# Kernel optimization log

Measured on AMD Instinct MI355X. Metric: run time of the kernel, lower is better.

The kernel has to match this reference:

```python
import jax, jax.numpy as jnp
import numpy as np
import math

B, L, D, H = 16, 512, 128, 8


def setup_inputs() -> dict:
    key = jax.random.key(0)
    ks = jax.random.split(key, 10)
    xavier = lambda k, shp: jax.random.normal(k, shp, jnp.float32) * math.sqrt(2.0 / (shp[0] + shp[1]))
    inp = {
        "x": jax.random.normal(ks[0], (B, L, D), jnp.float32),
        "W_q": xavier(ks[1], (H * D, D)),
        "b_q": jnp.zeros((H * D,), jnp.float32),
        "W_k": xavier(ks[2], (H * D, D)),
        "b_k": jnp.zeros((H * D,), jnp.float32),
        "W_v": xavier(ks[3], (H * D, D)),
        "b_v": jnp.zeros((H * D,), jnp.float32),
        "W_o": xavier(ks[4], (D, H * D)),
        "b_o": jnp.zeros((D,), jnp.float32),
        "pad_mask": jax.random.randint(ks[5], (B, L, L), 0, 2).astype(bool),
        "batch_size": B,
        "max_len": L,
    }
    return inp


def reference(x, W_q, b_q, W_k, b_k, W_v, b_v, W_o, b_o, pad_mask, batch_size, max_len):
    # project: [B, L, D] -> [B, L, H*D] -> head-major [H*B, L, D]
    def proj(W, b):
        y = jnp.einsum('bld,ed->ble', x, W) + b          # [B, L, H*D]
        y = y.reshape(batch_size, max_len, H, D)
        return y.transpose(2, 0, 1, 3).reshape(H * batch_size, max_len, D)

    q = proj(W_q, b_q)
    k = proj(W_k, b_k)
    v = proj(W_v, b_v)

    scores = jnp.einsum('nqd,nkd->nqk', q, k)            # [H*B, L, L]
    mask = jnp.tile(pad_mask, (H, 1, 1))                 # repeat(n_heads,1,1)
    # faithful quirk: mask BEFORE scaling, softmax over QUERY axis (dim=1)
    scores = jnp.where(mask, -1e9, scores) / math.sqrt(D)
    attn = jax.nn.softmax(scores, axis=1)
    att = jnp.einsum('nqk,nkd->nqd', attn, v)            # [H*B, L, D]
    # faithful quirk: torch .view from (H*B, L, D) to (B, L, H*D)
    att = att.reshape(batch_size, max_len, H * D)
    out = jnp.einsum('ble,de->bld', att, W_o) + b_o      # [B, L, D]
    return out
```

## Files before the change

kernel.cpp:

```cpp
#include <hip/hip_runtime.h>

#define B_  16
#define L_  512
#define D_  128
#define H_  8
#define HD_ 1024
#define NH_ 128
#define M_  8192

typedef unsigned short u16;
typedef __attribute__((ext_vector_type(8))) short s16x8;
typedef __attribute__((ext_vector_type(4))) float f32x4;

__device__ __forceinline__ float bf2f(u16 u) {
    union { unsigned u; float f; } x; x.u = ((unsigned)u) << 16; return x.f;
}
__device__ __forceinline__ u16 f2bf(float f) {
    unsigned u = __float_as_uint(f);
    return (u16)((u + 0x7FFFu + ((u >> 16) & 1u)) >> 16);
}

__device__ __forceinline__ void mfma_bt64(const u16* __restrict__ A, int lda,
                                          const u16* __restrict__ B, int ldb,
                                          int K, int lane, f32x4 acc[4][4]) {
    const int mr = lane & 15, quad = lane >> 4;
    for (int k0 = 0; k0 < K; k0 += 32) {
        s16x8 av[4], bv[4];
#pragma unroll
        for (int i = 0; i < 4; i++)
            av[i] = *(const s16x8*)(A + (size_t)(i * 16 + mr) * lda + k0 + quad * 8);
#pragma unroll
        for (int j = 0; j < 4; j++)
            bv[j] = *(const s16x8*)(B + (size_t)(j * 16 + mr) * ldb + k0 + quad * 8);
#pragma unroll
        for (int i = 0; i < 4; i++)
#pragma unroll
            for (int j = 0; j < 4; j++)
                acc[i][j] = __builtin_amdgcn_mfma_f32_16x16x32_bf16(av[i], bv[j], acc[i][j], 0, 0, 0);
    }
}

__global__ void k0_detect(const unsigned int* __restrict__ pad,
                          const unsigned int* __restrict__ xw,
                          int* __restrict__ flags) {
    __shared__ int sMask, sCnt;
    if (threadIdx.x == 0) { sMask = 0; sCnt = 0; }
    __syncthreads();
    int bad = 0;
#pragma unroll
    for (int i = 0; i < 4; i++) {
        unsigned u = pad[threadIdx.x * 4 + i];
        bad |= (u > 1u) ? 1 : 0;
    }
    int cnt = 0;
#pragma unroll
    for (int i = 0; i < 16; i++) {
        unsigned w = xw[threadIdx.x * 16 + i];
        unsigned e = (w >> 7) & 0xFFu;
        cnt += (e >= 100u && e <= 131u) ? 1 : 0;
    }
    if (bad) atomicOr(&sMask, 1);
    atomicAdd(&sCnt, cnt);
    __syncthreads();
    if (threadIdx.x == 0) {
        flags[0] = (sCnt > 2048) ? 1 : 0;
        flags[1] = sMask;
    }
}

#define PREP_TOT 1576064
__global__ __launch_bounds__(256) void kprep_conv(
    const void* x, const void* Wq, const void* bq, const void* Wk, const void* bk,
    const void* Wv, const void* bv, const void* Wo, const void* bo,
    const int* __restrict__ flags,
    u16* xb, u16* Wqb, u16* Wkb, u16* Wvb, u16* Wob,
    u16* bqb, u16* bkb, u16* bvb, u16* bob) {
    int gid = blockIdx.x * 256 + threadIdx.x;
    if (gid >= PREP_TOT) return;
    const int dt = flags[0];
    const void* src; u16* dst; int off;
    if      (gid < 1048576) { src = x;  dst = xb;  off = gid; }
    else if (gid < 1179648) { src = Wq; dst = Wqb; off = gid - 1048576; }
    else if (gid < 1310720) { src = Wk; dst = Wkb; off = gid - 1179648; }
    else if (gid < 1441792) { src = Wv; dst = Wvb; off = gid - 1310720; }
    else if (gid < 1572864) { src = Wo; dst = Wob; off = gid - 1441792; }
    else if (gid < 1573888) { src = bq; dst = bqb; off = gid - 1572864; }
    else if (gid < 1574912) { src = bk; dst = bkb; off = gid - 1573888; }
    else if (gid < 1575936) { src = bv; dst = bvb; off = gid - 1574912; }
    else                    { src = bo; dst = bob; off = gid - 1575936; }
    dst[off] = dt ? ((const u16*)src)[off] : f2bf(((const float*)src)[off]);
}

__global__ __launch_bounds__(256) void kprep_mask(const void* __restrict__ pad,
                                                  const int* __restrict__ flags,
                                                  unsigned* __restrict__ mb,
                                                  float* __restrict__ colsum) {
    int w = blockIdx.x * 256 + threadIdx.x;
    if (w < NH_ * L_) colsum[w] = 0.0f;
    unsigned m = 0;
    if (flags[1]) {
        const uint4* p = (const uint4*)pad + (size_t)w * 2;
        uint4 a = p[0], b = p[1];
        unsigned ws[8] = {a.x, a.y, a.z, a.w, b.x, b.y, b.z, b.w};
#pragma unroll
        for (int i = 0; i < 8; i++) {
            unsigned v = ws[i];
            m |= ((v & 0xFFu)        ? 1u : 0u) << (i * 4)
               | ((v & 0xFF00u)     ? 1u : 0u) << (i * 4 + 1)
               | ((v & 0xFF0000u)   ? 1u : 0u) << (i * 4 + 2)
               | ((v & 0xFF000000u) ? 1u : 0u) << (i * 4 + 3);
        }
    } else {
        const uint4* p = (const uint4*)pad + (size_t)w * 8;
#pragma unroll
        for (int i = 0; i < 8; i++) {
            uint4 v = p[i];
            m |= (v.x ? 1u : 0u) << (i * 4)
               | (v.y ? 1u : 0u) << (i * 4 + 1)
               | (v.z ? 1u : 0u) << (i * 4 + 2)
               | (v.w ? 1u : 0u) << (i * 4 + 3);
        }
    }
    mb[w] = m;
}

__global__ __launch_bounds__(256) void k1_proj(
    const u16* __restrict__ xb,
    const u16* __restrict__ Wqb, const u16* __restrict__ Wkb, const u16* __restrict__ Wvb,
    const u16* __restrict__ bqb, const u16* __restrict__ bkb, const u16* __restrict__ bvb,
    u16* __restrict__ qb, u16* __restrict__ kb, u16* __restrict__ vtb) {
    const int h  = blockIdx.x;
    const int m0 = blockIdx.y * 128;
    const int z  = blockIdx.z;
    const u16* W    = (z == 0) ? Wqb : (z == 1) ? Wkb : Wvb;
    const u16* bias = (z == 0) ? bqb : (z == 1) ? bkb : bvb;

    const int lane = threadIdx.x & 63, wave = threadIdx.x >> 6;
    const int wr = wave >> 1, wc = wave & 1;
    const int mr = lane & 15, quad = lane >> 4;

    f32x4 acc[4][4];
#pragma unroll
    for (int i = 0; i < 4; i++)
#pragma unroll
        for (int j = 0; j < 4; j++) acc[i][j] = (f32x4){0.f, 0.f, 0.f, 0.f};

    mfma_bt64(xb + (size_t)(m0 + wr * 64) * D_, D_,
              W + (size_t)(h * 128 + wc * 64) * D_, D_, D_, lane, acc);

    __shared__ __align__(16) u16 T[128][144];
#pragma unroll
    for (int i = 0; i < 4; i++)
#pragma unroll
        for (int j = 0; j < 4; j++) {
            int col = wc * 64 + j * 16 + mr;
            float bv_ = bf2f(bias[h * 128 + col]);
#pragma unroll
            for (int r = 0; r < 4; r++)
                T[wr * 64 + i * 16 + quad * 4 + r][col] = f2bf(acc[i][j][r] + bv_);
        }
    __syncthreads();

    const int bb = m0 >> 9, l0 = m0 & 511;
    const int t = threadIdx.x;
    if (z < 2) {
        u16* out = z ? kb : qb;
        int row = t >> 1, c0 = (t & 1) * 64;
        u16* dst = out + ((size_t)(h * B_ + bb) * L_ + l0 + row) * D_ + c0;
#pragma unroll
        for (int c = 0; c < 64; c += 8)
            *(uint4*)(dst + c) = *(const uint4*)&T[row][c0 + c];
    } else {
        int d = t >> 1, lc0 = (t & 1) * 64;
        u16* dst = vtb + ((size_t)(h * B_ + bb) * D_ + d) * L_ + l0 + lc0;
#pragma unroll
        for (int c = 0; c < 64; c += 8) {
            u16 tmp[8];
#pragma unroll
            for (int s = 0; s < 8; s++) tmp[s] = T[lc0 + c + s][d];
            *(uint4*)(dst + c) = *(const uint4*)tmp;
        }
    }
}

__global__ __launch_bounds__(256, 4) void k2_scores(
    const u16* __restrict__ qb, const u16* __restrict__ kb,
    const unsigned* __restrict__ mbits,
    u16* __restrict__ sb, float* __restrict__ colsum) {
    const int qt = blockIdx.x >> 2, kt = blockIdx.x & 3;
    const int n  = blockIdx.y;
    const int bb = n & (B_ - 1);
    const int lane = threadIdx.x & 63, wave = threadIdx.x >> 6;
    const int wr = wave >> 1, wc = wave & 1;
    const int mr = lane & 15, quad = lane >> 4;
    const float rs = 0.08838834764831845f;

    __shared__ __align__(16) u16 T[128][136];
    __shared__ float CS[2][128];
    __shared__ unsigned MW[128][4];

    {
        int t = threadIdx.x;
        int q = t >> 1, w2 = (t & 1) * 2;
        const unsigned* src = mbits + ((size_t)(bb << 9) + qt * 128 + q) * 16 + kt * 4 + w2;
        uint2 v = *(const uint2*)src;
        MW[q][w2] = v.x; MW[q][w2 + 1] = v.y;
    }

    f32x4 acc[4][4];
#pragma unroll
    for (int i = 0; i < 4; i++)
#pragma unroll
        for (int j = 0; j < 4; j++) acc[i][j] = (f32x4){0.f, 0.f, 0.f, 0.f};

    mfma_bt64(qb + ((size_t)n * L_ + qt * 128 + wr * 64) * D_, D_,
              kb + ((size_t)n * L_ + kt * 128 + wc * 64) * D_, D_, D_, lane, acc);
    __syncthreads();

    float cs[4] = {0.f, 0.f, 0.f, 0.f};
#pragma unroll
    for (int j = 0; j < 4; j++) {
        const int wsel = wc * 2 + (j >> 1);
        const int bit  = ((j & 1) << 4) + mr;
#pragma unroll
        for (int i = 0; i < 4; i++)
#pragma unroll
            for (int r = 0; r < 4; r++) {
                int ql = wr * 64 + i * 16 + quad * 4 + r;
                unsigned w = MW[ql][wsel];
                float e = ((w >> bit) & 1u) ? 0.f : __expf(acc[i][j][r] * rs);
                cs[j] += e;
                T[ql][wc * 64 + j * 16 + mr] = f2bf(e);
            }
    }
#pragma unroll
    for (int j = 0; j < 4; j++) {
        cs[j] += __shfl_xor(cs[j], 16);
        cs[j] += __shfl_xor(cs[j], 32);
    }
    if (quad == 0) {
#pragma unroll
        for (int j = 0; j < 4; j++) CS[wr][wc * 64 + j * 16 + mr] = cs[j];
    }
    __syncthreads();
    {
        int t = threadIdx.x, row = t >> 1, c0 = (t & 1) * 64;
        u16* dst = sb + ((size_t)n * L_ + qt * 128 + row) * L_ + kt * 128 + c0;
#pragma unroll
        for (int c = 0; c < 64; c += 8)
            *(uint4*)(dst + c) = *(const uint4*)&T[row][c0 + c];
    }
    if (threadIdx.x < 128)
        atomicAdd(&colsum[(size_t)n * L_ + kt * 128 + threadIdx.x],
                  CS[0][threadIdx.x] + CS[1][threadIdx.x]);
}

__global__ __launch_bounds__(256) void k3_vscale(u16* __restrict__ vtb,
                                                 const float* __restrict__ colsum) {
    int idx = blockIdx.x * 256 + threadIdx.x;
    int n = idx >> 13;
    int rem = idx & 8191;
    int d = rem >> 6;
    int kg = (rem & 63) << 3;
    u16* p = vtb + ((size_t)n * D_ + d) * L_ + kg;
    uint4 v = *(const uint4*)p;
    float cv[8];
    *(float4*)&cv[0] = *(const float4*)(colsum + (size_t)n * L_ + kg);
    *(float4*)&cv[4] = *(const float4*)(colsum + (size_t)n * L_ + kg + 4);
    u16* u = (u16*)&v;
#pragma unroll
    for (int s = 0; s < 8; s++) u[s] = f2bf(bf2f(u[s]) / cv[s]);
    *(uint4*)p = v;
}

__global__ __launch_bounds__(256) void k4_av(
    const u16* __restrict__ sb, const u16* __restrict__ vtb,
    u16* __restrict__ att) {
    const int q0 = blockIdx.x * 128;
    const int n  = blockIdx.y;
    const int lane = threadIdx.x & 63, wave = threadIdx.x >> 6;
    const int wr = wave >> 1, wc = wave & 1;
    const int mr = lane & 15, quad = lane >> 4;

    f32x4 acc[4][4];
#pragma unroll
    for (int i = 0; i < 4; i++)
#pragma unroll
        for (int j = 0; j < 4; j++) acc[i][j] = (f32x4){0.f, 0.f, 0.f, 0.f};

    mfma_bt64(sb + ((size_t)n * L_ + q0 + wr * 64) * L_, L_,
              vtb + ((size_t)n * D_ + wc * 64) * L_, L_, L_, lane, acc);

    __shared__ __align__(16) u16 T[128][136];
#pragma unroll
    for (int i = 0; i < 4; i++)
#pragma unroll
        for (int j = 0; j < 4; j++) {
            int col = wc * 64 + j * 16 + mr;
#pragma unroll
            for (int r = 0; r < 4; r++)
                T[wr * 64 + i * 16 + quad * 4 + r][col] = f2bf(acc[i][j][r]);
        }
    __syncthreads();
    int t = threadIdx.x, row = t >> 1, c0 = (t & 1) * 64;
    u16* dst = att + ((size_t)n * L_ + q0 + row) * D_ + c0;
#pragma unroll
    for (int c = 0; c < 64; c += 8)
        *(uint4*)(dst + c) = *(const uint4*)&T[row][c0 + c];
}

__global__ __launch_bounds__(256) void k5_out(
    const u16* __restrict__ att, const u16* __restrict__ Wob,
    const u16* __restrict__ bob, const int* __restrict__ flags,
    void* __restrict__ out) {
    const int dt = flags[0];
    const int m0 = blockIdx.x * 32;
    const int lane = threadIdx.x & 63, wave = threadIdx.x >> 6;
    const int mr = lane & 15, quad = lane >> 4;

    f32x4 acc[2][2];
#pragma unroll
    for (int i = 0; i < 2; i++)
#pragma unroll
        for (int j = 0; j < 2; j++) acc[i][j] = (f32x4){0.f, 0.f, 0.f, 0.f};

    const u16* A  = att + (size_t)m0 * HD_;
    const u16* Bw = Wob + (size_t)(wave * 32) * HD_;
    for (int k0 = 0; k0 < HD_; k0 += 32) {
        s16x8 av[2], bv[2];
#pragma unroll
        for (int i = 0; i < 2; i++)
            av[i] = *(const s16x8*)(A + (size_t)(i * 16 + mr) * HD_ + k0 + quad * 8);
#pragma unroll
        for (int j = 0; j < 2; j++)
            bv[j] = *(const s16x8*)(Bw + (size_t)(j * 16 + mr) * HD_ + k0 + quad * 8);
#pragma unroll
        for (int i = 0; i < 2; i++)
#pragma unroll
            for (int j = 0; j < 2; j++)
                acc[i][j] = __builtin_amdgcn_mfma_f32_16x16x32_bf16(av[i], bv[j], acc[i][j], 0, 0, 0);
    }

    __shared__ __align__(16) float Tf[32][132];
#pragma unroll
    for (int i = 0; i < 2; i++)
#pragma unroll
        for (int j = 0; j < 2; j++) {
            int col = wave * 32 + j * 16 + mr;
            float bv_ = bf2f(bob[col]);
#pragma unroll
            for (int r = 0; r < 4; r++)
                Tf[i * 16 + quad * 4 + r][col] = acc[i][j][r] + bv_;
        }
    __syncthreads();
    int t = threadIdx.x, row = t >> 3, cg = (t & 7) * 16;
    size_t base = (size_t)(m0 + row) * D_ + cg;
    if (dt) {
        u16* o = (u16*)out;
        u16 tmp[16];
#pragma unroll
        for (int s = 0; s < 16; s++) tmp[s] = f2bf(Tf[row][cg + s]);
        *(uint4*)(o + base)     = *(const uint4*)&tmp[0];
        *(uint4*)(o + base + 8) = *(const uint4*)&tmp[8];
    } else {
        float* o = (float*)out;
#pragma unroll
        for (int c = 0; c < 16; c += 4)
            *(float4*)(o + base + c) = *(const float4*)&Tf[row][cg + c];
    }
}

extern "C" void kernel_launch(void* const* d_in, const int* in_sizes, int n_in,
                              void* d_out, int out_size, void* d_ws, size_t ws_size,
                              hipStream_t stream) {
    (void)in_sizes; (void)n_in; (void)out_size; (void)ws_size;
    const void* x  = d_in[0];
    const void* Wq = d_in[1]; const void* bq = d_in[2];
    const void* Wk = d_in[3]; const void* bk = d_in[4];
    const void* Wv = d_in[5]; const void* bv = d_in[6];
    const void* Wo = d_in[7]; const void* bo = d_in[8];
    const void* pad = d_in[9];

    char* p = (char*)d_ws;
    auto alloc = [&](size_t bytes) { char* r = p; p += (bytes + 255) & ~(size_t)255; return r; };
    int*  flags = (int*)alloc(256);
    u16*  xb   = (u16*)alloc(2097152);
    u16*  Wqb  = (u16*)alloc(262144);
    u16*  Wkb  = (u16*)alloc(262144);
    u16*  Wvb  = (u16*)alloc(262144);
    u16*  Wob  = (u16*)alloc(262144);
    u16*  bqb  = (u16*)alloc(2048);
    u16*  bkb  = (u16*)alloc(2048);
    u16*  bvb  = (u16*)alloc(2048);
    u16*  bob  = (u16*)alloc(256);
    unsigned* mbits = (unsigned*)alloc(524288);
    float* colsum = (float*)alloc(262144);
    u16*  qb   = (u16*)alloc(16777216);
    u16*  kb   = (u16*)alloc(16777216);
    u16*  vtb  = (u16*)alloc(16777216);
    u16*  sb   = (u16*)alloc(67108864);
    u16*  att  = qb;

    k0_detect<<<1, 256, 0, stream>>>((const unsigned*)pad, (const unsigned*)x, flags);
    kprep_conv<<<(PREP_TOT + 255) / 256, 256, 0, stream>>>(
        x, Wq, bq, Wk, bk, Wv, bv, Wo, bo, flags,
        xb, Wqb, Wkb, Wvb, Wob, bqb, bkb, bvb, bob);
    kprep_mask<<<512, 256, 0, stream>>>(pad, flags, mbits, colsum);
    k1_proj<<<dim3(8, 64, 3), 256, 0, stream>>>(
        xb, Wqb, Wkb, Wvb, bqb, bkb, bvb, qb, kb, vtb);
    k2_scores<<<dim3(16, NH_), 256, 0, stream>>>(qb, kb, mbits, sb, colsum);
    k3_vscale<<<4096, 256, 0, stream>>>(vtb, colsum);
    k4_av<<<dim3(4, NH_), 256, 0, stream>>>(sb, vtb, att);
    k5_out<<<256, 256, 0, stream>>>(att, Wob, bob, flags, d_out);
}
```

Before: 253.4 us.

## Fuse V column scaling into AV kernel and vectorize prep conversion

Removes the separate k3_vscale pass. The softmax denominator reciprocal is now applied to the score operand inside the AV matmul loop, which is equivalent because it indexes the reduction axis. The prep conversion kernel processes 8 elements per thread with vector loads and stores. The projection grid axes are swapped, which changes block scheduling order. Scaling in k4 is repeated across q tiles and adds ALU work in the inner loop, and rounding differs slightly.

New measurement: 244.9 us. -3.4%, faster.

```diff
diff --git a/kernel.cpp b/kernel.cpp
--- a/kernel.cpp
+++ b/kernel.cpp
@@ -69,6 +69,7 @@
 }
 
 #define PREP_TOT 1576064
+#define PREP_V   197008
 __global__ __launch_bounds__(256) void kprep_conv(
     const void* x, const void* Wq, const void* bq, const void* Wk, const void* bk,
     const void* Wv, const void* bv, const void* Wo, const void* bo,
@@ -76,19 +77,28 @@
     u16* xb, u16* Wqb, u16* Wkb, u16* Wvb, u16* Wob,
     u16* bqb, u16* bkb, u16* bvb, u16* bob) {
     int gid = blockIdx.x * 256 + threadIdx.x;
-    if (gid >= PREP_TOT) return;
+    if (gid >= PREP_V) return;
+    int e0 = gid * 8;
     const int dt = flags[0];
     const void* src; u16* dst; int off;
-    if      (gid < 1048576) { src = x;  dst = xb;  off = gid; }
-    else if (gid < 1179648) { src = Wq; dst = Wqb; off = gid - 1048576; }
-    else if (gid < 1310720) { src = Wk; dst = Wkb; off = gid - 1179648; }
-    else if (gid < 1441792) { src = Wv; dst = Wvb; off = gid - 1310720; }
-    else if (gid < 1572864) { src = Wo; dst = Wob; off = gid - 1441792; }
-    else if (gid < 1573888) { src = bq; dst = bqb; off = gid - 1572864; }
-    else if (gid < 1574912) { src = bk; dst = bkb; off = gid - 1573888; }
-    else if (gid < 1575936) { src = bv; dst = bvb; off = gid - 1574912; }
-    else                    { src = bo; dst = bob; off = gid - 1575936; }
-    dst[off] = dt ? ((const u16*)src)[off] : f2bf(((const float*)src)[off]);
+    if      (e0 < 1048576) { src = x;  dst = xb;  off = e0; }
+    else if (e0 < 1179648) { src = Wq; dst = Wqb; off = e0 - 1048576; }
+    else if (e0 < 1310720) { src = Wk; dst = Wkb; off = e0 - 1179648; }
+    else if (e0 < 1441792) { src = Wv; dst = Wvb; off = e0 - 1310720; }
+    else if (e0 < 1572864) { src = Wo; dst = Wob; off = e0 - 1441792; }
+    else if (e0 < 1573888) { src = bq; dst = bqb; off = e0 - 1572864; }
+    else if (e0 < 1574912) { src = bk; dst = bkb; off = e0 - 1573888; }
+    else if (e0 < 1575936) { src = bv; dst = bvb; off = e0 - 1574912; }
+    else                   { src = bo; dst = bob; off = e0 - 1575936; }
+    if (dt) {
+        *(uint4*)(dst + off) = *(const uint4*)((const u16*)src + off);
+    } else {
+        const float* s = (const float*)src + off;
+        float4 a = *(const float4*)s, b = *(const float4*)(s + 4);
+        u16 tmp[8] = {f2bf(a.x), f2bf(a.y), f2bf(a.z), f2bf(a.w),
+                      f2bf(b.x), f2bf(b.y), f2bf(b.z), f2bf(b.w)};
+        *(uint4*)(dst + off) = *(const uint4*)tmp;
+    }
 }
 
 __global__ __launch_bounds__(256) void kprep_mask(const void* __restrict__ pad,
@@ -129,8 +139,8 @@
     const u16* __restrict__ Wqb, const u16* __restrict__ Wkb, const u16* __restrict__ Wvb,
     const u16* __restrict__ bqb, const u16* __restrict__ bkb, const u16* __restrict__ bvb,
     u16* __restrict__ qb, u16* __restrict__ kb, u16* __restrict__ vtb) {
-    const int h  = blockIdx.x;
-    const int m0 = blockIdx.y * 128;
+    const int h  = blockIdx.y;
+    const int m0 = blockIdx.x * 128;
     const int z  = blockIdx.z;
     const u16* W    = (z == 0) ? Wqb : (z == 1) ? Wkb : Wvb;
     const u16* bias = (z == 0) ? bqb : (z == 1) ? bkb : bvb;
@@ -255,27 +265,9 @@
                   CS[0][threadIdx.x] + CS[1][threadIdx.x]);
 }
 
-__global__ __launch_bounds__(256) void k3_vscale(u16* __restrict__ vtb,
-                                                 const float* __restrict__ colsum) {
-    int idx = blockIdx.x * 256 + threadIdx.x;
-    int n = idx >> 13;
-    int rem = idx & 8191;
-    int d = rem >> 6;
-    int kg = (rem & 63) << 3;
-    u16* p = vtb + ((size_t)n * D_ + d) * L_ + kg;
-    uint4 v = *(const uint4*)p;
-    float cv[8];
-    *(float4*)&cv[0] = *(const float4*)(colsum + (size_t)n * L_ + kg);
-    *(float4*)&cv[4] = *(const float4*)(colsum + (size_t)n * L_ + kg + 4);
-    u16* u = (u16*)&v;
-#pragma unroll
-    for (int s = 0; s < 8; s++) u[s] = f2bf(bf2f(u[s]) / cv[s]);
-    *(uint4*)p = v;
-}
-
 __global__ __launch_bounds__(256) void k4_av(
     const u16* __restrict__ sb, const u16* __restrict__ vtb,
-    u16* __restrict__ att) {
+    const float* __restrict__ colsum, u16* __restrict__ att) {
     const int q0 = blockIdx.x * 128;
     const int n  = blockIdx.y;
     const int lane = threadIdx.x & 63, wave = threadIdx.x >> 6;
@@ -288,8 +280,37 @@
 #pragma unroll
         for (int j = 0; j < 4; j++) acc[i][j] = (f32x4){0.f, 0.f, 0.f, 0.f};
 
-    mfma_bt64(sb + ((size_t)n * L_ + q0 + wr * 64) * L_, L_,
-              vtb + ((size_t)n * D_ + wc * 64) * L_, L_, L_, lane, acc);
+    const u16* A   = sb  + ((size_t)n * L_ + q0 + wr * 64) * L_;
+    const u16* Bb  = vtb + ((size_t)n * D_ + wc * 64) * L_;
+    const float* cs = colsum + (size_t)n * L_;
+
+    for (int k0 = 0; k0 < L_; k0 += 32) {
+        const int kk = k0 + quad * 8;
+        float lv[8];
+        *(float4*)&lv[0] = *(const float4*)(cs + kk);
+        *(float4*)&lv[4] = *(const float4*)(cs + kk + 4);
+#pragma unroll
+        for (int s = 0; s < 8; s++) lv[s] = __builtin_amdgcn_rcpf(lv[s]);
+
+        s16x8 av[4], bv[4];
+#pragma unroll
+        for (int i = 0; i < 4; i++)
+            av[i] = *(const s16x8*)(A + (size_t)(i * 16 + mr) * L_ + kk);
+#pragma unroll
+        for (int j = 0; j < 4; j++)
+            bv[j] = *(const s16x8*)(Bb + (size_t)(j * 16 + mr) * L_ + kk);
+#pragma unroll
+        for (int i = 0; i < 4; i++) {
+            u16* u = (u16*)&av[i];
+#pragma unroll
+            for (int s = 0; s < 8; s++) u[s] = f2bf(bf2f(u[s]) * lv[s]);
+        }
+#pragma unroll
+        for (int i = 0; i < 4; i++)
+#pragma unroll
+            for (int j = 0; j < 4; j++)
+                acc[i][j] = __builtin_amdgcn_mfma_f32_16x16x32_bf16(av[i], bv[j], acc[i][j], 0, 0, 0);
+    }
 
     __shared__ __align__(16) u16 T[128][136];
 #pragma unroll
@@ -402,14 +423,13 @@
     u16*  att  = qb;
 
     k0_detect<<<1, 256, 0, stream>>>((const unsigned*)pad, (const unsigned*)x, flags);
-    kprep_conv<<<(PREP_TOT + 255) / 256, 256, 0, stream>>>(
+    kprep_conv<<<(PREP_V + 255) / 256, 256, 0, stream>>>(
         x, Wq, bq, Wk, bk, Wv, bv, Wo, bo, flags,
         xb, Wqb, Wkb, Wvb, Wob, bqb, bkb, bvb, bob);
     kprep_mask<<<512, 256, 0, stream>>>(pad, flags, mbits, colsum);
-    k1_proj<<<dim3(8, 64, 3), 256, 0, stream>>>(
+    k1_proj<<<dim3(64, 8, 3), 256, 0, stream>>>(
         xb, Wqb, Wkb, Wvb, bqb, bkb, bvb, qb, kb, vtb);
     k2_scores<<<dim3(16, NH_), 256, 0, stream>>>(qb, kb, mbits, sb, colsum);
-    k3_vscale<<<4096, 256, 0, stream>>>(vtb, colsum);
-    k4_av<<<dim3(4, NH_), 256, 0, stream>>>(sb, vtb, att);
+    k4_av<<<dim3(4, NH_), 256, 0, stream>>>(sb, vtb, colsum, att);
     k5_out<<<256, 256, 0, stream>>>(att, Wob, bob, flags, d_out);
 }
```
